# Kernel optimization log

Measured on AMD Instinct MI355X. Metric: run time of the kernel, lower is better.

The kernel has to match this reference:

```python
import jax, jax.numpy as jnp
import numpy as np

N_EMBED = 1024
HEAD_SIZE = 64
NUM_HEADS = 16
BLOCK_SIZE = 2048


def setup_inputs() -> dict:
    key = jax.random.key(0)
    kx, kq, kk, kv, kp, kb = jax.random.split(key, 6)
    B, T = 4, 2048
    d = N_EMBED
    hd = NUM_HEADS * HEAD_SIZE
    s = 1.0 / np.sqrt(d)
    return {
        "x": jax.random.normal(kx, (B, T, d), dtype=jnp.float32),
        "Wq": jax.random.uniform(kq, (d, hd), dtype=jnp.float32, minval=-s, maxval=s),
        "Wk": jax.random.uniform(kk, (d, hd), dtype=jnp.float32, minval=-s, maxval=s),
        "Wv": jax.random.uniform(kv, (d, hd), dtype=jnp.float32, minval=-s, maxval=s),
        "Wp": jax.random.uniform(kp, (hd, d), dtype=jnp.float32, minval=-s, maxval=s),
        "bp": jax.random.uniform(kb, (d,), dtype=jnp.float32, minval=-s, maxval=s),
    }


def reference(x, Wq, Wk, Wv, Wp, bp):
    B, T, _ = x.shape
    H, hs = NUM_HEADS, HEAD_SIZE
    # project and split heads: [B, H, T, hs]
    q = (x @ Wq).reshape(B, T, H, hs).transpose(0, 2, 1, 3)
    k = (x @ Wk).reshape(B, T, H, hs).transpose(0, 2, 1, 3)
    v = (x @ Wv).reshape(B, T, H, hs).transpose(0, 2, 1, 3)
    # full T x T causal scores (faithful to non-flash original)
    wei = jnp.einsum("bhqd,bhkd->bhqk", q, k) * (hs ** -0.5)
    causal = jnp.tril(jnp.ones((T, T), dtype=bool))
    wei = jnp.where(causal[None, None], wei, -jnp.inf)
    wei = jax.nn.softmax(wei, axis=-1)
    out = jnp.einsum("bhqk,bhkd->bhqd", wei, v)
    out = out.transpose(0, 2, 1, 3).reshape(B, T, H * hs)
    return out @ Wp + bp
```

## Files before the change

kernel.cpp:

```cpp
#include <hip/hip_runtime.h>
#include <hip/hip_bf16.h>

#define BATCH 4
#define SEQ   2048
#define DMODEL 1024
#define NHEAD 16
#define HS    64
#define MROWS (BATCH*SEQ)
#define KDIM  DMODEL
#define NDIM  DMODEL

typedef short bf16x8 __attribute__((ext_vector_type(8)));
typedef float f32x4  __attribute__((ext_vector_type(4)));
typedef int   i32x2  __attribute__((ext_vector_type(2)));
typedef unsigned u32x4 __attribute__((ext_vector_type(4)));

#if __has_builtin(__builtin_amdgcn_exp2f)
#define EXP2(x) __builtin_amdgcn_exp2f(x)
#else
#define EXP2(x) exp2f(x)
#endif

static __device__ __forceinline__ unsigned short f2bf(float f) {
    union { float f; unsigned int u; } v; v.f = f;
    unsigned int r = (v.u + 0x7fffu + ((v.u >> 16) & 1u)) >> 16;
    return (unsigned short)r;
}

static __device__ __forceinline__ unsigned int pk_bf16(float a, float b) {
    union { __hip_bfloat162 h; unsigned int u; } c;
    c.h = __float22bfloat162_rn(make_float2(a, b));
    return c.u;
}

static __device__ __forceinline__ void pl32swap(unsigned &a, unsigned &b) {
#if __has_builtin(__builtin_amdgcn_permlane32_swap)
    i32x2 r = __builtin_amdgcn_permlane32_swap((int)a, (int)b, false, false);
    a = (unsigned)r[0]; b = (unsigned)r[1];
#else
    asm volatile("v_permlane32_swap_b32 %0, %1" : "+v"(a), "+v"(b));
#endif
}
static __device__ __forceinline__ void pl16swap(unsigned &a, unsigned &b) {
#if __has_builtin(__builtin_amdgcn_permlane16_swap)
    i32x2 r = __builtin_amdgcn_permlane16_swap((int)a, (int)b, false, false);
    a = (unsigned)r[0]; b = (unsigned)r[1];
#else
    asm volatile("v_permlane16_swap_b32 %0, %1" : "+v"(a), "+v"(b));
#endif
}

static __device__ __forceinline__ void gl2lds16(const void* g, void* l) {
    __builtin_amdgcn_global_load_lds((const __attribute__((address_space(1))) unsigned int*)g,
                                     (__attribute__((address_space(3))) unsigned int*)l, 16, 0, 0);
}

__global__ __launch_bounds__(256) void cvt_bf16(const float* __restrict__ in,
                                                unsigned short* __restrict__ out) {
    int i = blockIdx.x * 256 + threadIdx.x;
    float4 v = ((const float4*)in)[i];
    ushort4 o;
    o.x = f2bf(v.x); o.y = f2bf(v.y); o.z = f2bf(v.z); o.w = f2bf(v.w);
    ((ushort4*)out)[i] = o;
}

__global__ __launch_bounds__(256) void transpose_cvt4(const float* __restrict__ s0, const float* __restrict__ s1,
                                                      const float* __restrict__ s2, const float* __restrict__ s3,
                                                      unsigned short* __restrict__ d0, unsigned short* __restrict__ d1,
                                                      unsigned short* __restrict__ d2, unsigned short* __restrict__ d3) {
    const float* in; unsigned short* out;
    switch (blockIdx.z) {
        case 0:  in = s0; out = d0; break;
        case 1:  in = s1; out = d1; break;
        case 2:  in = s2; out = d2; break;
        default: in = s3; out = d3; break;
    }
    __shared__ float t[32][33];
    int tx = threadIdx.x, ty = threadIdx.y;
    int x = blockIdx.x * 32 + tx;
    #pragma unroll
    for (int i = 0; i < 4; ++i) {
        int y = blockIdx.y * 32 + ty + i * 8;
        t[ty + i * 8][tx] = in[(size_t)y * 1024 + x];
    }
    __syncthreads();
    int x2 = blockIdx.y * 32 + tx;
    #pragma unroll
    for (int i = 0; i < 4; ++i) {
        int y2 = blockIdx.x * 32 + ty + i * 8;
        out[(size_t)y2 * 1024 + x2] = f2bf(t[tx][ty + i * 8]);
    }
}

#define GEMM_DECLS                                                                      \
    __shared__ __align__(16) short Sm[2 * 128 * 64];                                    \
    short* As = Sm;                                                                     \
    short* Bs = Sm + 128 * 64;                                                          \
    const int tid  = threadIdx.x;                                                       \
    const int lane = tid & 63;                                                          \
    const int w    = tid >> 6;                                                          \
    const int wm   = w >> 1, wn = w & 1;                                                \
    const int cc   = lane & 15, quad = lane >> 4;                                       \
    const int bn   = blockIdx.x;                                                        \
    const int bm   = blockIdx.y;                                                        \
    f32x4 acc[4][4] = {};

#define GEMM_KLOOP(TRANS)                                                               \
    {                                                                                   \
    const unsigned short* Ab = A  + (size_t)bm * 128 * KDIM;                            \
    const unsigned short* Bb = Bt + (size_t)bn * 128 * KDIM;                            \
    for (int kb = 0; kb < KDIM; kb += 64) {                                             \
        __syncthreads();                                                                \
        _Pragma("unroll")                                                               \
        for (int i = 0; i < 4; ++i) {                                                   \
            int S = (i * 4 + w) * 64 + lane;                                            \
            int r = S >> 3, g = (S & 7) ^ (r & 7);                                      \
            gl2lds16(Ab + (size_t)r * KDIM + kb + g * 8, (void*)&As[S * 8]);            \
            gl2lds16(Bb + (size_t)r * KDIM + kb + g * 8, (void*)&Bs[S * 8]);            \
        }                                                                               \
        asm volatile("s_waitcnt vmcnt(0)");                                             \
        __syncthreads();                                                                \
        _Pragma("unroll")                                                               \
        for (int kh = 0; kh < 2; ++kh) {                                                \
            bf16x8 xf[4], wf[4];                                                        \
            _Pragma("unroll")                                                           \
            for (int mt = 0; mt < 4; ++mt) {                                            \
                int r = wm * 64 + mt * 16 + cc;                                         \
                xf[mt] = *(const bf16x8*)&As[r * 64 + ((kh * 4 + quad) ^ (r & 7)) * 8]; \
            }                                                                           \
            _Pragma("unroll")                                                           \
            for (int nt = 0; nt < 4; ++nt) {                                            \
                int r = wn * 64 + nt * 16 + cc;                                         \
                wf[nt] = *(const bf16x8*)&Bs[r * 64 + ((kh * 4 + quad) ^ (r & 7)) * 8]; \
            }                                                                           \
            _Pragma("unroll")                                                           \
            for (int mt = 0; mt < 4; ++mt)                                              \
                _Pragma("unroll")                                                       \
                for (int nt = 0; nt < 4; ++nt)                                          \
                    acc[mt][nt] = (TRANS)                                               \
                      ? __builtin_amdgcn_mfma_f32_16x16x32_bf16(wf[nt], xf[mt], acc[mt][nt], 0, 0, 0) \
                      : __builtin_amdgcn_mfma_f32_16x16x32_bf16(xf[mt], wf[nt], acc[mt][nt], 0, 0, 0); \
        }                                                                               \
    }                                                                                   \
    }

__global__ __launch_bounds__(256, 3) void gemm_qkv(const unsigned short* __restrict__ A,
                                                   const unsigned short* __restrict__ Bt,
                                                   unsigned short* __restrict__ Qo,
                                                   unsigned short* __restrict__ Ko,
                                                   unsigned short* __restrict__ Vo) {
    GEMM_DECLS
    if (bn < 16) {
        GEMM_KLOOP(1)
        const bool isK = bn >= 8;
        const float scale = isK ? 1.0f : 0.125f * 1.44269504f;
        unsigned short* outp = isK ? Ko : Qo;
        __syncthreads();
        #pragma unroll
        for (int mt = 0; mt < 4; ++mt) {
            #pragma unroll
            for (int nt = 0; nt < 4; ++nt) {
                int t  = wm * 64 + mt * 16 + cc;
                int e0 = wn * 64 + nt * 16 + quad * 4;
                uint2 pu;
                pu.x = pk_bf16(acc[mt][nt][0] * scale, acc[mt][nt][1] * scale);
                pu.y = pk_bf16(acc[mt][nt][2] * scale, acc[mt][nt][3] * scale);
                int sp = (e0 >> 2) ^ (t & 31);
                *(uint2*)&Sm[t * 128 + sp * 4] = pu;
            }
        }
        __syncthreads();
        const int h0 = (bn & 7) * 2;
        const int b  = bm >> 4;
        const int t0 = (bm & 15) * 128;
        #pragma unroll
        for (int i = 0; i < 8; ++i) {
            int s = i * 256 + tid;
            int t = s >> 4, g = s & 15;
            int sp0 = (2 * g)     ^ (t & 31);
            int sp1 = (2 * g + 1) ^ (t & 31);
            uint2 lo = *(const uint2*)&Sm[t * 128 + sp0 * 4];
            uint2 hi = *(const uint2*)&Sm[t * 128 + sp1 * 4];
            int h = h0 + (g >> 3), e = (g & 7) * 8;
            size_t addr = ((size_t)(b * NHEAD + h) * SEQ + t0 + t) * HS + e;
            uint4 u; u.x = lo.x; u.y = lo.y; u.z = hi.x; u.w = hi.y;
            *(uint4*)&outp[addr] = u;
        }
    } else {
        GEMM_KLOOP(0)
        __syncthreads();
        #pragma unroll
        for (int mt = 0; mt < 4; ++mt) {
            #pragma unroll
            for (int nt = 0; nt < 4; ++nt) {
                int n    = wn * 64 + nt * 16 + cc;
                int slot = wm * 16 + mt * 4 + quad;
                int sp   = slot ^ (n & 31);
                uint2 pu;
                pu.x = pk_bf16(acc[mt][nt][0], acc[mt][nt][1]);
                pu.y = pk_bf16(acc[mt][nt][2], acc[mt][nt][3]);
                *(uint2*)&Sm[n * 128 + sp * 4] = pu;
            }
        }
        __syncthreads();
        const int h0 = (bn & 7) * 2;
        const int b  = bm >> 4;
        const int t0 = (bm & 15) * 128;
        #pragma unroll
        for (int i = 0; i < 8; ++i) {
            int s = i * 256 + tid;
            int n = s >> 4, g = s & 15;
            int sp0 = (2 * g)     ^ (n & 31);
            int sp1 = (2 * g + 1) ^ (n & 31);
            uint2 lo = *(const uint2*)&Sm[n * 128 + sp0 * 4];
            uint2 hi = *(const uint2*)&Sm[n * 128 + sp1 * 4];
            int h = h0 + (n >> 6), e = n & 63;
            size_t addr = ((size_t)((b * NHEAD + h) * HS + e)) * SEQ + t0 + g * 8;
            uint4 u; u.x = lo.x; u.y = lo.y; u.z = hi.x; u.w = hi.y;
            *(uint4*)&Vo[addr] = u;
        }
    }
}

__global__ __launch_bounds__(256, 3) void gemm_proj(const unsigned short* __restrict__ A,
                                                    const unsigned short* __restrict__ Bt,
                                                    float* __restrict__ Cout,
                                                    const float* __restrict__ bias) {
    GEMM_DECLS
    GEMM_KLOOP(0)
    #pragma unroll
    for (int mt = 0; mt < 4; ++mt) {
        #pragma unroll
        for (int nt = 0; nt < 4; ++nt) {
            f32x4 a = acc[mt][nt];
            int gn  = bn * 128 + wn * 64 + nt * 16 + cc;
            int gm0 = bm * 128 + wm * 64 + mt * 16 + quad * 4;
            #pragma unroll
            for (int r = 0; r < 4; ++r)
                Cout[(size_t)(gm0 + r) * NDIM + gn] = a[r] + bias[gn];
        }
    }
}

__global__ __launch_bounds__(256, 3) void flash_attn(const unsigned short* __restrict__ Q,
                                                     const unsigned short* __restrict__ K,
                                                     const unsigned short* __restrict__ Vt,
                                                     unsigned short* __restrict__ O) {
    __shared__ __align__(16) short Ks[128 * 64];
    __shared__ __align__(16) short Vs[64 * 128];

    const int tid  = threadIdx.x;
    const int lane = tid & 63;
    const int w    = tid >> 6;
    const int cc   = lane & 15, quad = lane >> 4;
    const int bh   = blockIdx.x;
    const int qblk = ((int)gridDim.y - 1 - (int)blockIdx.y) * 128;
    const int b    = bh >> 4, h = bh & 15;

    const unsigned short* Qb = Q  + (size_t)bh * SEQ * HS;
    const unsigned short* Kb = K  + (size_t)bh * SEQ * HS;
    const unsigned short* Vb = Vt + (size_t)bh * HS * SEQ;

    bf16x8 qf[2][2];
    #pragma unroll
    for (int qt = 0; qt < 2; ++qt) {
        int qg = qblk + w * 32 + qt * 16;
        const unsigned short* qp = Qb + (size_t)(qg + cc) * HS;
        qf[qt][0] = *(const bf16x8*)(qp + quad * 8);
        qf[qt][1] = *(const bf16x8*)(qp + 32 + quad * 8);
    }

    bf16x8 onesv;
    #pragma unroll
    for (int j = 0; j < 8; ++j) onesv[j] = (short)0x3F80;

    f32x4 o[2][4] = {};
    f32x4 lacc[2] = {};
    const f32x4 zero = {};

#define STAGE_KV(kb_)                                                                   \
    _Pragma("unroll")                                                                   \
    for (int i = 0; i < 4; ++i) {                                                       \
        int S = (i * 4 + w) * 64 + lane;                                                \
        {                                                 \
            int r = S >> 3, g = (S & 7) ^ (r & 7);                                      \
            gl2lds16(Kb + (size_t)((kb_) + r) * HS + g * 8, (void*)&Ks[S * 8]);         \
        }                                                                               \
        {                                                  \
            int d = S >> 4, g = (S & 15) ^ (d & 15);                                    \
            gl2lds16(Vb + (size_t)d * SEQ + (kb_) + g * 8, (void*)&Vs[S * 8]);          \
        }                                                                               \
    }

#define QK_GROUP(g_, sdst)                                                              \
    {                                                                                   \
        _Pragma("unroll")                                                               \
        for (int ktl = 0; ktl < 2; ++ktl) {                                             \
            int r = ((g_) * 2 + ktl) * 16 + cc;                                         \
            bf16x8 kf0 = *(const bf16x8*)&Ks[r * 64 + ((quad)     ^ (r & 7)) * 8];      \
            bf16x8 kf1 = *(const bf16x8*)&Ks[r * 64 + ((4 + quad) ^ (r & 7)) * 8];      \
            sdst[0][ktl] = __builtin_amdgcn_mfma_f32_16x16x32_bf16(kf0, qf[0][0], zero,        0, 0, 0); \
            sdst[0][ktl] = __builtin_amdgcn_mfma_f32_16x16x32_bf16(kf1, qf[0][1], sdst[0][ktl], 0, 0, 0); \
            sdst[1][ktl] = __builtin_amdgcn_mfma_f32_16x16x32_bf16(kf0, qf[1][0], zero,        0, 0, 0); \
            sdst[1][ktl] = __builtin_amdgcn_mfma_f32_16x16x32_bf16(kf1, qf[1][1], sdst[1][ktl], 0, 0, 0); \
        }                                                                               \
    }

#define SMPV(g_, s_)                                                                    \
    {                                                                                   \
        bf16x8 pb[2];                                                                   \
        _Pragma("unroll")                                                               \
        for (int qt = 0; qt < 2; ++qt) {                                                \
            const int qg = qblk + w * 32 + qt * 16;                                     \
            if (kb + (g_) * 32 + 31 > qg) {                \
                _Pragma("unroll")                                                       \
                for (int ktl = 0; ktl < 2; ++ktl)                                       \
                    _Pragma("unroll")                                                   \
                    for (int r = 0; r < 4; ++r)                                         \
                        if (kb + ((g_) * 2 + ktl) * 16 + quad * 4 + r > qg + cc)        \
                            s_[qt][ktl][r] = -1e30f;                                    \
            }                                                                           \
            _Pragma("unroll")                                                           \
            for (int ktl = 0; ktl < 2; ++ktl) {                                         \
                s_[qt][ktl][0] = EXP2(s_[qt][ktl][0]);                                  \
                s_[qt][ktl][1] = EXP2(s_[qt][ktl][1]);                                  \
                s_[qt][ktl][2] = EXP2(s_[qt][ktl][2]);                                  \
                s_[qt][ktl][3] = EXP2(s_[qt][ktl][3]);                                  \
            }                                                                           \
            unsigned a0 = pk_bf16(s_[qt][0][0], s_[qt][0][1]);                          \
            unsigned a1 = pk_bf16(s_[qt][0][2], s_[qt][0][3]);                          \
            unsigned b0 = pk_bf16(s_[qt][1][0], s_[qt][1][1]);                          \
            unsigned b1 = pk_bf16(s_[qt][1][2], s_[qt][1][3]);                          \
            pl32swap(a0, b0); pl16swap(a0, b0);     \
            pl32swap(a1, b1); pl16swap(a1, b1);     \
            u32x4 pw; pw[0] = a0; pw[1] = a1; pw[2] = b0; pw[3] = b1;                   \
            pb[qt] = __builtin_bit_cast(bf16x8, pw);                                    \
        }                                                                               \
        lacc[0] = __builtin_amdgcn_mfma_f32_16x16x32_bf16(onesv, pb[0], lacc[0], 0, 0, 0); \
        lacc[1] = __builtin_amdgcn_mfma_f32_16x16x32_bf16(onesv, pb[1], lacc[1], 0, 0, 0); \
        _Pragma("unroll")                                                               \
        for (int nt = 0; nt < 4; ++nt) {                                                \
            int d = nt * 16 + cc;                                                       \
            bf16x8 vf = *(const bf16x8*)&Vs[d * 128 + (((g_) * 4 + quad) ^ (d & 15)) * 8]; \
            o[0][nt] = __builtin_amdgcn_mfma_f32_16x16x32_bf16(vf, pb[0], o[0][nt], 0, 0, 0); \
            o[1][nt] = __builtin_amdgcn_mfma_f32_16x16x32_bf16(vf, pb[1], o[1][nt], 0, 0, 0); \
        }                                                                               \
    }

    const int trips = qblk / 128 + 1;
    for (int it = 0; it < trips; ++it) {
        const int kb = it * 128;

        STAGE_KV(kb)
        asm volatile("s_waitcnt vmcnt(0)" ::: "memory");
        __builtin_amdgcn_s_barrier();
        __builtin_amdgcn_sched_barrier(0);

        const int gact = (kb == qblk) ? (w + 1) : 4;

        f32x4 s0[2][2], s1[2][2];
        QK_GROUP(0, s0)
        if (1 < gact) QK_GROUP(1, s1)
        SMPV(0, s0)
        if (2 < gact) QK_GROUP(2, s0)
        if (1 < gact) SMPV(1, s1)
        if (3 < gact) QK_GROUP(3, s1)
        if (2 < gact) SMPV(2, s0)
        if (3 < gact) SMPV(3, s1)

        __builtin_amdgcn_sched_barrier(0);
        __builtin_amdgcn_s_barrier();
    }

    #pragma unroll
    for (int qt = 0; qt < 2; ++qt) {
        int qg = qblk + w * 32 + qt * 16;
        float inv = 1.0f / lacc[qt][0];
        size_t base = ((size_t)b * SEQ + qg + cc) * DMODEL + h * HS;
        #pragma unroll
        for (int nt = 0; nt < 4; ++nt) {
            ushort4 u;
            u.x = f2bf(o[qt][nt][0] * inv);
            u.y = f2bf(o[qt][nt][1] * inv);
            u.z = f2bf(o[qt][nt][2] * inv);
            u.w = f2bf(o[qt][nt][3] * inv);
            *(ushort4*)&O[base + nt * 16 + quad * 4] = u;
        }
    }
}

extern "C" void kernel_launch(void* const* d_in, const int* in_sizes, int n_in,
                              void* d_out, int out_size, void* d_ws, size_t ws_size,
                              hipStream_t stream) {
    const float* x  = (const float*)d_in[0];
    const float* Wq = (const float*)d_in[1];
    const float* Wk = (const float*)d_in[2];
    const float* Wv = (const float*)d_in[3];
    const float* Wp = (const float*)d_in[4];
    const float* bp = (const float*)d_in[5];
    float* out = (float*)d_out;

    char* ws = (char*)d_ws;
    unsigned short* xb    = (unsigned short*)(ws);
    unsigned short* wqkvt = (unsigned short*)(ws + (16u << 20));
    unsigned short* wpt   = (unsigned short*)(ws + (22u << 20));
    unsigned short* qws   = (unsigned short*)(ws + (24u << 20));
    unsigned short* kws   = (unsigned short*)(ws + (40u << 20));
    unsigned short* vtws  = (unsigned short*)(ws + (56u << 20));
    unsigned short* attn  = (unsigned short*)(ws + (72u << 20));

    cvt_bf16<<<MROWS * DMODEL / 1024, 256, 0, stream>>>(x, xb);

    transpose_cvt4<<<dim3(32, 32, 4), dim3(32, 8), 0, stream>>>(
        Wq, Wk, Wv, Wp, wqkvt, wqkvt + (1u << 20), wqkvt + (2u << 20), wpt);

    gemm_qkv<<<dim3(24, MROWS / 128), 256, 0, stream>>>(xb, wqkvt, qws, kws, vtws);

    flash_attn<<<dim3(BATCH * NHEAD, SEQ / 128), 256, 0, stream>>>(qws, kws, vtws, attn);

    gemm_proj<<<dim3(NDIM / 128, MROWS / 128), 256, 0, stream>>>(attn, wpt, out, bp);
}
```

Measured before the change: 229.0 us.

## Pair complementary causal query blocks per workgroup to balance load and share K/V tiles

```diff
diff --git a/kernel.cpp b/kernel.cpp
--- a/kernel.cpp
+++ b/kernel.cpp
@@ -242,7 +242,7 @@
     }
 }
 
-__global__ __launch_bounds__(256, 3) void flash_attn(const unsigned short* __restrict__ Q,
+__global__ __launch_bounds__(256, 2) void flash_attn(const unsigned short* __restrict__ Q,
                                                      const unsigned short* __restrict__ K,
                                                      const unsigned short* __restrict__ Vt,
                                                      unsigned short* __restrict__ O) {
@@ -254,28 +254,32 @@
     const int w    = tid >> 6;
     const int cc   = lane & 15, quad = lane >> 4;
     const int bh   = blockIdx.x;
-    const int qblk = ((int)gridDim.y - 1 - (int)blockIdx.y) * 128;
+    const int j    = blockIdx.y;
+    const int qa   = j * 128;
+    const int qb   = (SEQ / 128 - 1 - j) * 128;
     const int b    = bh >> 4, h = bh & 15;
 
     const unsigned short* Qb = Q  + (size_t)bh * SEQ * HS;
     const unsigned short* Kb = K  + (size_t)bh * SEQ * HS;
     const unsigned short* Vb = Vt + (size_t)bh * HS * SEQ;
 
-    bf16x8 qf[2][2];
+    bf16x8 qfa[2][2], qfb[2][2];
     #pragma unroll
     for (int qt = 0; qt < 2; ++qt) {
-        int qg = qblk + w * 32 + qt * 16;
-        const unsigned short* qp = Qb + (size_t)(qg + cc) * HS;
-        qf[qt][0] = *(const bf16x8*)(qp + quad * 8);
-        qf[qt][1] = *(const bf16x8*)(qp + 32 + quad * 8);
+        const unsigned short* qpa = Qb + (size_t)(qa + w * 32 + qt * 16 + cc) * HS;
+        qfa[qt][0] = *(const bf16x8*)(qpa + quad * 8);
+        qfa[qt][1] = *(const bf16x8*)(qpa + 32 + quad * 8);
+        const unsigned short* qpb = Qb + (size_t)(qb + w * 32 + qt * 16 + cc) * HS;
+        qfb[qt][0] = *(const bf16x8*)(qpb + quad * 8);
+        qfb[qt][1] = *(const bf16x8*)(qpb + 32 + quad * 8);
     }
 
     bf16x8 onesv;
     #pragma unroll
-    for (int j = 0; j < 8; ++j) onesv[j] = (short)0x3F80;
-
-    f32x4 o[2][4] = {};
-    f32x4 lacc[2] = {};
+    for (int jj = 0; jj < 8; ++jj) onesv[jj] = (short)0x3F80;
+
+    f32x4 oa[2][4] = {}, ob[2][4] = {};
+    f32x4 lacca[2] = {}, laccb[2] = {};
     const f32x4 zero = {};
 
 #define STAGE_KV(kb_)                                                                   \
@@ -292,26 +296,26 @@
         }                                                                               \
     }
 
-#define QK_GROUP(g_, sdst)                                                              \
+#define QK_GROUP(g_, sdst, qf_)                                                         \
     {                                                                                   \
         _Pragma("unroll")                                                               \
         for (int ktl = 0; ktl < 2; ++ktl) {                                             \
             int r = ((g_) * 2 + ktl) * 16 + cc;                                         \
             bf16x8 kf0 = *(const bf16x8*)&Ks[r * 64 + ((quad)     ^ (r & 7)) * 8];      \
             bf16x8 kf1 = *(const bf16x8*)&Ks[r * 64 + ((4 + quad) ^ (r & 7)) * 8];      \
-            sdst[0][ktl] = __builtin_amdgcn_mfma_f32_16x16x32_bf16(kf0, qf[0][0], zero,        0, 0, 0); \
-            sdst[0][ktl] = __builtin_amdgcn_mfma_f32_16x16x32_bf16(kf1, qf[0][1], sdst[0][ktl], 0, 0, 0); \
-            sdst[1][ktl] = __builtin_amdgcn_mfma_f32_16x16x32_bf16(kf0, qf[1][0], zero,        0, 0, 0); \
-            sdst[1][ktl] = __builtin_amdgcn_mfma_f32_16x16x32_bf16(kf1, qf[1][1], sdst[1][ktl], 0, 0, 0); \
-        }                                                                               \
-    }
-
-#define SMPV(g_, s_)                                                                    \
+            sdst[0][ktl] = __builtin_amdgcn_mfma_f32_16x16x32_bf16(kf0, qf_[0][0], zero,         0, 0, 0); \
+            sdst[0][ktl] = __builtin_amdgcn_mfma_f32_16x16x32_bf16(kf1, qf_[0][1], sdst[0][ktl], 0, 0, 0); \
+            sdst[1][ktl] = __builtin_amdgcn_mfma_f32_16x16x32_bf16(kf0, qf_[1][0], zero,         0, 0, 0); \
+            sdst[1][ktl] = __builtin_amdgcn_mfma_f32_16x16x32_bf16(kf1, qf_[1][1], sdst[1][ktl], 0, 0, 0); \
+        }                                                                               \
+    }
+
+#define SMPV(g_, s_, qblk_, o_, lacc_)                                                  \
     {                                                                                   \
         bf16x8 pb[2];                                                                   \
         _Pragma("unroll")                                                               \
         for (int qt = 0; qt < 2; ++qt) {                                                \
-            const int qg = qblk + w * 32 + qt * 16;                                     \
+            const int qg = (qblk_) + w * 32 + qt * 16;                                  \
             if (kb + (g_) * 32 + 31 > qg) {                \
                 _Pragma("unroll")                                                       \
                 for (int ktl = 0; ktl < 2; ++ktl)                                       \
@@ -336,18 +340,18 @@
             u32x4 pw; pw[0] = a0; pw[1] = a1; pw[2] = b0; pw[3] = b1;                   \
             pb[qt] = __builtin_bit_cast(bf16x8, pw);                                    \
         }                                                                               \
-        lacc[0] = __builtin_amdgcn_mfma_f32_16x16x32_bf16(onesv, pb[0], lacc[0], 0, 0, 0); \
-        lacc[1] = __builtin_amdgcn_mfma_f32_16x16x32_bf16(onesv, pb[1], lacc[1], 0, 0, 0); \
+        lacc_[0] = __builtin_amdgcn_mfma_f32_16x16x32_bf16(onesv, pb[0], lacc_[0], 0, 0, 0); \
+        lacc_[1] = __builtin_amdgcn_mfma_f32_16x16x32_bf16(onesv, pb[1], lacc_[1], 0, 0, 0); \
         _Pragma("unroll")                                                               \
         for (int nt = 0; nt < 4; ++nt) {                                                \
             int d = nt * 16 + cc;                                                       \
             bf16x8 vf = *(const bf16x8*)&Vs[d * 128 + (((g_) * 4 + quad) ^ (d & 15)) * 8]; \
-            o[0][nt] = __builtin_amdgcn_mfma_f32_16x16x32_bf16(vf, pb[0], o[0][nt], 0, 0, 0); \
-            o[1][nt] = __builtin_amdgcn_mfma_f32_16x16x32_bf16(vf, pb[1], o[1][nt], 0, 0, 0); \
-        }                                                                               \
-    }
-
-    const int trips = qblk / 128 + 1;
+            o_[0][nt] = __builtin_amdgcn_mfma_f32_16x16x32_bf16(vf, pb[0], o_[0][nt], 0, 0, 0); \
+            o_[1][nt] = __builtin_amdgcn_mfma_f32_16x16x32_bf16(vf, pb[1], o_[1][nt], 0, 0, 0); \
+        }                                                                               \
+    }
+
+    const int trips = qb / 128 + 1;
     for (int it = 0; it < trips; ++it) {
         const int kb = it * 128;
 
@@ -356,17 +360,26 @@
         __builtin_amdgcn_s_barrier();
         __builtin_amdgcn_sched_barrier(0);
 
-        const int gact = (kb == qblk) ? (w + 1) : 4;
+        const int gb = (kb == qb) ? (w + 1) : 4;
+        const int ga = (kb == qa) ? (w + 1) : (kb < qa ? 4 : 0);
 
         f32x4 s0[2][2], s1[2][2];
-        QK_GROUP(0, s0)
-        if (1 < gact) QK_GROUP(1, s1)
-        SMPV(0, s0)
-        if (2 < gact) QK_GROUP(2, s0)
-        if (1 < gact) SMPV(1, s1)
-        if (3 < gact) QK_GROUP(3, s1)
-        if (2 < gact) SMPV(2, s0)
-        if (3 < gact) SMPV(3, s1)
+        QK_GROUP(0, s0, qfb)
+        if (1 < gb) QK_GROUP(1, s1, qfb)
+        SMPV(0, s0, qb, ob, laccb)
+        if (2 < gb) QK_GROUP(2, s0, qfb)
+        if (1 < gb) SMPV(1, s1, qb, ob, laccb)
+        if (3 < gb) QK_GROUP(3, s1, qfb)
+        if (2 < gb) SMPV(2, s0, qb, ob, laccb)
+        if (0 < ga) QK_GROUP(0, s0, qfa)
+        if (3 < gb) SMPV(3, s1, qb, ob, laccb)
+        if (1 < ga) QK_GROUP(1, s1, qfa)
+        if (0 < ga) SMPV(0, s0, qa, oa, lacca)
+        if (2 < ga) QK_GROUP(2, s0, qfa)
+        if (1 < ga) SMPV(1, s1, qa, oa, lacca)
+        if (3 < ga) QK_GROUP(3, s1, qfa)
+        if (2 < ga) SMPV(2, s0, qa, oa, lacca)
+        if (3 < ga) SMPV(3, s1, qa, oa, lacca)
 
         __builtin_amdgcn_sched_barrier(0);
         __builtin_amdgcn_s_barrier();
@@ -374,17 +387,33 @@
 
     #pragma unroll
     for (int qt = 0; qt < 2; ++qt) {
-        int qg = qblk + w * 32 + qt * 16;
-        float inv = 1.0f / lacc[qt][0];
-        size_t base = ((size_t)b * SEQ + qg + cc) * DMODEL + h * HS;
-        #pragma unroll
-        for (int nt = 0; nt < 4; ++nt) {
-            ushort4 u;
-            u.x = f2bf(o[qt][nt][0] * inv);
-            u.y = f2bf(o[qt][nt][1] * inv);
-            u.z = f2bf(o[qt][nt][2] * inv);
-            u.w = f2bf(o[qt][nt][3] * inv);
-            *(ushort4*)&O[base + nt * 16 + quad * 4] = u;
+        {
+            int qg = qa + w * 32 + qt * 16;
+            float inv = 1.0f / lacca[qt][0];
+            size_t base = ((size_t)b * SEQ + qg + cc) * DMODEL + h * HS;
+            #pragma unroll
+            for (int nt = 0; nt < 4; ++nt) {
+                ushort4 u;
+                u.x = f2bf(oa[qt][nt][0] * inv);
+                u.y = f2bf(oa[qt][nt][1] * inv);
+                u.z = f2bf(oa[qt][nt][2] * inv);
+                u.w = f2bf(oa[qt][nt][3] * inv);
+                *(ushort4*)&O[base + nt * 16 + quad * 4] = u;
+            }
+        }
+        {
+            int qg = qb + w * 32 + qt * 16;
+            float inv = 1.0f / laccb[qt][0];
+            size_t base = ((size_t)b * SEQ + qg + cc) * DMODEL + h * HS;
+            #pragma unroll
+            for (int nt = 0; nt < 4; ++nt) {
+                ushort4 u;
+                u.x = f2bf(ob[qt][nt][0] * inv);
+                u.y = f2bf(ob[qt][nt][1] * inv);
+                u.z = f2bf(ob[qt][nt][2] * inv);
+                u.w = f2bf(ob[qt][nt][3] * inv);
+                *(ushort4*)&O[base + nt * 16 + quad * 4] = u;
+            }
         }
     }
 }
@@ -416,7 +445,7 @@
 
     gemm_qkv<<<dim3(24, MROWS / 128), 256, 0, stream>>>(xb, wqkvt, qws, kws, vtws);
 
-    flash_attn<<<dim3(BATCH * NHEAD, SEQ / 128), 256, 0, stream>>>(qws, kws, vtws, attn);
+    flash_attn<<<dim3(BATCH * NHEAD, SEQ / 256), 256, 0, stream>>>(qws, kws, vtws, attn);
 
     gemm_proj<<<dim3(NDIM / 128, MROWS / 128), 256, 0, stream>>>(attn, wpt, out, bp);
 }
```

New measurement: 230.4 us. Within noise of the previous version (+0.6%).
